# Kernel optimization log

Hardware: AMD Instinct MI355X
Metric: run time of the kernel (lower is better)

## Reference

```python
import jax, jax.numpy as jnp
import numpy as np

NUM_AGENTS = 1000
N_ACTIONS = 16
HIDDEN = 256
COMM_STEPS = 4
B, M = 1024, 64


def setup_inputs() -> dict:
    key = jax.random.key(0)
    ks = jax.random.split(key, 8)
    agent_ids = jax.random.randint(ks[0], (B, M), 0, NUM_AGENTS)
    emb = jax.random.normal(ks[1], (NUM_AGENTS, HIDDEN), dtype=jnp.float32) * 0.1
    s1 = 1.0 / np.sqrt(3 * HIDDEN)
    W1 = jax.random.uniform(ks[2], (3 * HIDDEN, HIDDEN), jnp.float32, -s1, s1)
    b1 = jax.random.uniform(ks[3], (HIDDEN,), jnp.float32, -s1, s1)
    s2 = 1.0 / np.sqrt(HIDDEN)
    W2 = jax.random.uniform(ks[4], (HIDDEN, HIDDEN), jnp.float32, -s2, s2)
    b2 = jax.random.uniform(ks[5], (HIDDEN,), jnp.float32, -s2, s2)
    Wd = jax.random.uniform(ks[6], (HIDDEN, N_ACTIONS), jnp.float32, -s2, s2)
    bd = jax.random.uniform(ks[7], (N_ACTIONS,), jnp.float32, -s2, s2)
    return {"agent_ids": agent_ids, "emb": emb, "W1": W1, "b1": b1,
            "W2": W2, "b2": b2, "Wd": Wd, "bd": bd}


def reference(agent_ids, emb, W1, b1, W2, b2, Wd, bd):
    # h0: (B, M, H) embedding lookup
    h0 = emb[agent_ids]
    h = h0
    m = agent_ids.shape[1]
    inv = 1.0 / (m - 1)
    for _ in range(COMM_STEPS):
        # mean of other agents' hidden states: c_j = (sum_k h_k - h_j)/(M-1)
        c = (jnp.sum(h, axis=1, keepdims=True) - h) * inv
        x = jnp.concatenate([h, c, h0], axis=-1)  # (B, M, 3H)
        delta = jax.nn.relu(jnp.einsum('bmi,ih->bmh', x, W1) + b1)
        delta = jnp.einsum('bmi,ih->bmh', delta, W2) + b2
        h = h + delta  # residual (use_skip=True)
    logits = jnp.einsum('bmh,ha->bma', h, Wd) + bd
    return logits
```

## Files before the change

kernel.cpp:

```cpp
#include <hip/hip_runtime.h>

#define HID 256
#define NB 1024
#define NACT 16
#define HSTRIDE 528

typedef __bf16 bf16x8 __attribute__((ext_vector_type(8)));
typedef float  f32x4  __attribute__((ext_vector_type(4)));

#define HA_LO   33792
#define HB_SZ   67584
#define S_OFF   135168
#define LDS_TOT 137216

#define PREP_N (4 * 65536 + 4096)

__device__ __forceinline__ unsigned short f2bf(float x) {
    union { __bf16 b; unsigned short u; } v; v.b = (__bf16)x; return v.u;
}
__device__ __forceinline__ float bf2f(unsigned short u) {
    union { unsigned short u; __bf16 b; } v; v.u = u; return (float)v.b;
}
__device__ __forceinline__ float b2f_lo(unsigned v) { return bf2f((unsigned short)(v & 0xffffu)); }
__device__ __forceinline__ float b2f_hi(unsigned v) { return bf2f((unsigned short)(v >> 16)); }
__device__ __forceinline__ unsigned pack2(float a, float b) {
    return (unsigned)f2bf(a) | ((unsigned)f2bf(b) << 16);
}

__global__ __launch_bounds__(256) void prep_k(const float* __restrict__ W1,
                                              const float* __restrict__ W2,
                                              const float* __restrict__ Wd,
                                              unsigned short* __restrict__ WAh, unsigned short* __restrict__ WAl,
                                              unsigned short* __restrict__ WHh, unsigned short* __restrict__ WHl,
                                              unsigned short* __restrict__ WBh, unsigned short* __restrict__ WBl,
                                              unsigned short* __restrict__ WCh, unsigned short* __restrict__ WCl,
                                              unsigned short* __restrict__ WDh, unsigned short* __restrict__ WDl) {
    int i = blockIdx.x * 256 + threadIdx.x;
    const float inv = 1.0f / 63.0f;
    if (i < 4 * 65536) {
        int mat = i >> 16, j = i & 65535;
        int kq = j >> 13, r = j & 8191;
        int nb = r >> 9, r2 = r & 511;
        int l = r2 >> 3, e = r2 & 7;
        int n = nb * 16 + (l & 15);
        int k = kq * 32 + (l >> 4) * 8 + e;
        float val;
        if (mat == 0)      val = W1[k * 256 + n] - inv * W1[(256 + k) * 256 + n];
        else if (mat == 1) val = W1[(512 + k) * 256 + n];
        else if (mat == 2) val = W2[k * 256 + n];
        else               val = inv * W1[(256 + k) * 256 + n];
        unsigned short hi = f2bf(val);
        unsigned short lo = f2bf(val - bf2f(hi));
        if (mat == 0)      { WAh[j] = hi; WAl[j] = lo; }
        else if (mat == 1) { WHh[j] = hi; WHl[j] = lo; }
        else if (mat == 2) { WBh[j] = hi; WBl[j] = lo; }
        else               { WCh[j] = hi; WCl[j] = lo; }
    } else if (i < PREP_N) {
        int j = i - 4 * 65536, a = j >> 8, k = j & 255;
        float val = Wd[k * 16 + a];
        unsigned short hi = f2bf(val);
        WDh[j] = hi; WDl[j] = f2bf(val - bf2f(hi));
    }
}

__device__ __forceinline__ void kloopL2(const unsigned short* __restrict__ Wfh,
                                        const unsigned short* __restrict__ Wfl,
                                        const char* hA, f32x4 (&acc)[4][2],
                                        size_t lbase, int l15, int g)
{
    #pragma unroll 2
    for (int kq = 0; kq < 8; ++kq) {
        const int cb = kq * 64 + g * 16;
        bf16x8 ah[4], al[4];
        #pragma unroll
        for (int mt = 0; mt < 4; ++mt) {
            int rb = (mt * 16 + l15) * HSTRIDE;
            ah[mt] = *(const bf16x8*)(hA + rb + cb);
            al[mt] = *(const bf16x8*)(hA + HA_LO + rb + cb);
        }
        const size_t kb = (size_t)kq * 8192 + lbase;
        #pragma unroll
        for (int nt = 0; nt < 2; ++nt) {
            bf16x8 bh = *(const bf16x8*)(Wfh + kb + nt * 512);
            bf16x8 bl = *(const bf16x8*)(Wfl + kb + nt * 512);
            #pragma unroll
            for (int mt = 0; mt < 4; ++mt) {
                acc[mt][nt] = __builtin_amdgcn_mfma_f32_16x16x32_bf16(bh, ah[mt], acc[mt][nt], 0, 0, 0);
                acc[mt][nt] = __builtin_amdgcn_mfma_f32_16x16x32_bf16(bh, al[mt], acc[mt][nt], 0, 0, 0);
                acc[mt][nt] = __builtin_amdgcn_mfma_f32_16x16x32_bf16(bl, ah[mt], acc[mt][nt], 0, 0, 0);
            }
        }
    }
}

__global__ __launch_bounds__(1024, 1) void fused_all(
    const int* __restrict__ ids, const float* __restrict__ emb,
    const unsigned short* __restrict__ WAh, const unsigned short* __restrict__ WAl,
    const unsigned short* __restrict__ WHh, const unsigned short* __restrict__ WHl,
    const unsigned short* __restrict__ WBh, const unsigned short* __restrict__ WBl,
    const unsigned short* __restrict__ WCh, const unsigned short* __restrict__ WCl,
    const unsigned short* __restrict__ WDh, const unsigned short* __restrict__ WDl,
    const float* __restrict__ b1, const float* __restrict__ b2,
    const float* __restrict__ bd, float* __restrict__ out)
{
    __shared__ __align__(16) char lds[LDS_TOT];
    const int tid = threadIdx.x;
    const int lane = tid & 63;
    const int w = tid >> 6;
    const int wcol = w & 7;
    const int batch = w >> 3;
    const int l15 = lane & 15, g = lane >> 4;
    const size_t rowbase = (size_t)blockIdx.x * 128 + batch * 64;
    char* hA = lds + batch * HB_SZ;
    float* Sf = (float*)(lds + S_OFF + batch * 1024);
    const size_t lbase = ((size_t)(wcol * 2) * 64 + lane) * 8;
    const int cb0 = wcol * 32 + g * 4;

    {
        int r = tid >> 3, c0 = (tid & 7) * 32;
        const float4* src = (const float4*)(emb + (size_t)ids[(size_t)blockIdx.x * 128 + r] * HID + c0);
        char* dh = lds + (r >> 6) * HB_SZ + (r & 63) * HSTRIDE + c0 * 2;
        #pragma unroll
        for (int j = 0; j < 8; ++j) {
            float4 v = src[j];
            unsigned short h0 = f2bf(v.x), h1 = f2bf(v.y), h2 = f2bf(v.z), h3 = f2bf(v.w);
            unsigned short q0 = f2bf(v.x - bf2f(h0)), q1 = f2bf(v.y - bf2f(h1)),
                           q2 = f2bf(v.z - bf2f(h2)), q3 = f2bf(v.w - bf2f(h3));
            *(uint2*)(dh + j * 8) = make_uint2((unsigned)h0 | ((unsigned)h1 << 16),
                                               (unsigned)h2 | ((unsigned)h3 << 16));
            *(uint2*)(dh + HA_LO + j * 8) = make_uint2((unsigned)q0 | ((unsigned)q1 << 16),
                                                       (unsigned)q2 | ((unsigned)q3 << 16));
        }
    }
    __syncthreads();

    if (tid < 512) {
        int b = tid >> 8, col = tid & 255;
        const char* hb = lds + b * HB_SZ;
        float ssum = 0.f;
        #pragma unroll 8
        for (int m = 0; m < 64; ++m) {
            int byte = m * HSTRIDE + col * 2;
            ssum += bf2f(*(const unsigned short*)(hb + byte))
                  + bf2f(*(const unsigned short*)(hb + HA_LO + byte));
        }
        ((float*)(lds + S_OFF + b * 1024))[col] = ssum;
    }
    __syncthreads();

    f32x4 b1v0 = *(const f32x4*)(b1 + cb0);
    f32x4 b1v1 = *(const f32x4*)(b1 + cb0 + 16);
    f32x4 b2v0 = *(const f32x4*)(b2 + cb0);
    f32x4 b2v1 = *(const f32x4*)(b2 + cb0 + 16);

    f32x4 acc[4][2], u0r[4][2];
    #pragma unroll
    for (int mt = 0; mt < 4; ++mt)
        #pragma unroll
        for (int nt = 0; nt < 2; ++nt) acc[mt][nt] = (f32x4){0.f, 0.f, 0.f, 0.f};

    kloopL2(WHh, WHl, hA, acc, lbase, l15, g);
    #pragma unroll
    for (int mt = 0; mt < 4; ++mt) {
        u0r[mt][0] = acc[mt][0] + b1v0;
        u0r[mt][1] = acc[mt][1] + b1v1;
    }

    for (int s = 0; s < 4; ++s) {
        f32x4 tacc[2];
        tacc[0] = tacc[1] = (f32x4){0.f, 0.f, 0.f, 0.f};
        #pragma unroll 2
        for (int kq = 0; kq < 8; ++kq) {
            const float* sp = Sf + kq * 32 + g * 8;
            f32x4 sa = *(const f32x4*)sp;
            f32x4 sb = *(const f32x4*)(sp + 4);
            unsigned sh[4], sl[4];
            sh[0] = pack2(sa[0], sa[1]); sh[1] = pack2(sa[2], sa[3]);
            sh[2] = pack2(sb[0], sb[1]); sh[3] = pack2(sb[2], sb[3]);
            sl[0] = pack2(sa[0] - b2f_lo(sh[0]), sa[1] - b2f_hi(sh[0]));
            sl[1] = pack2(sa[2] - b2f_lo(sh[1]), sa[3] - b2f_hi(sh[1]));
            sl[2] = pack2(sb[0] - b2f_lo(sh[2]), sb[1] - b2f_hi(sh[2]));
            sl[3] = pack2(sb[2] - b2f_lo(sh[3]), sb[3] - b2f_hi(sh[3]));
            bf16x8 shv = *(const bf16x8*)sh;
            bf16x8 slv = *(const bf16x8*)sl;
            const size_t kb = (size_t)kq * 8192 + lbase;
            #pragma unroll
            for (int nt = 0; nt < 2; ++nt) {
                bf16x8 wch = *(const bf16x8*)(WCh + kb + nt * 512);
                bf16x8 wcl = *(const bf16x8*)(WCl + kb + nt * 512);
                tacc[nt] = __builtin_amdgcn_mfma_f32_16x16x32_bf16(wch, shv, tacc[nt], 0, 0, 0);
                tacc[nt] = __builtin_amdgcn_mfma_f32_16x16x32_bf16(wch, slv, tacc[nt], 0, 0, 0);
                tacc[nt] = __builtin_amdgcn_mfma_f32_16x16x32_bf16(wcl, shv, tacc[nt], 0, 0, 0);
            }
        }

        #pragma unroll
        for (int mt = 0; mt < 4; ++mt)
            #pragma unroll
            for (int nt = 0; nt < 2; ++nt)
                acc[mt][nt] = u0r[mt][nt] + tacc[nt];
        kloopL2(WAh, WAl, hA, acc, lbase, l15, g);

        __syncthreads();
        #pragma unroll
        for (int mt = 0; mt < 4; ++mt)
            #pragma unroll
            for (int nt = 0; nt < 2; ++nt) {
                int byte = (mt * 16 + l15) * HSTRIDE + (cb0 + nt * 16) * 2;
                uint2 ph = *(const uint2*)(hA + byte);
                uint2 pl = *(const uint2*)(hA + HA_LO + byte);
                f32x4 hres;
                hres[0] = b2f_lo(ph.x) + b2f_lo(pl.x);
                hres[1] = b2f_hi(ph.x) + b2f_hi(pl.x);
                hres[2] = b2f_lo(ph.y) + b2f_lo(pl.y);
                hres[3] = b2f_hi(ph.y) + b2f_hi(pl.y);
                f32x4 av = acc[mt][nt];
                float a0 = fmaxf(av[0], 0.f), a1 = fmaxf(av[1], 0.f);
                float a2 = fmaxf(av[2], 0.f), a3 = fmaxf(av[3], 0.f);
                unsigned h01 = pack2(a0, a1), h23 = pack2(a2, a3);
                float r0 = a0 - b2f_lo(h01);
                float r1 = a1 - b2f_hi(h01);
                float r2 = a2 - b2f_lo(h23);
                float r3 = a3 - b2f_hi(h23);
                *(uint2*)(hA + byte) = make_uint2(h01, h23);
                *(uint2*)(hA + HA_LO + byte) = make_uint2(pack2(r0, r1), pack2(r2, r3));
                acc[mt][nt] = hres + (nt ? b2v1 : b2v0);
            }
        __syncthreads();

        kloopL2(WBh, WBl, hA, acc, lbase, l15, g);

        __syncthreads();
        #pragma unroll
        for (int mt = 0; mt < 4; ++mt)
            #pragma unroll
            for (int nt = 0; nt < 2; ++nt) {
                int byte = (mt * 16 + l15) * HSTRIDE + (cb0 + nt * 16) * 2;
                f32x4 av = acc[mt][nt];
                unsigned h01 = pack2(av[0], av[1]), h23 = pack2(av[2], av[3]);
                float r0 = av[0] - b2f_lo(h01);
                float r1 = av[1] - b2f_hi(h01);
                float r2 = av[2] - b2f_lo(h23);
                float r3 = av[3] - b2f_hi(h23);
                *(uint2*)(hA + byte) = make_uint2(h01, h23);
                *(uint2*)(hA + HA_LO + byte) = make_uint2(pack2(r0, r1), pack2(r2, r3));
            }
        if (s < 3) {
            #pragma unroll
            for (int nt = 0; nt < 2; ++nt) {
                f32x4 cs = (acc[0][nt] + acc[1][nt]) + (acc[2][nt] + acc[3][nt]);
                #pragma unroll
                for (int d = 1; d < 16; d <<= 1) {
                    cs[0] += __shfl_xor(cs[0], d);
                    cs[1] += __shfl_xor(cs[1], d);
                    cs[2] += __shfl_xor(cs[2], d);
                    cs[3] += __shfl_xor(cs[3], d);
                }
                if (l15 == 0) *(f32x4*)(Sf + cb0 + nt * 16) = cs;
            }
        }
        __syncthreads();
    }

    if (wcol < 4) {
        f32x4 dacc = (f32x4){0.f, 0.f, 0.f, 0.f};
        #pragma unroll 2
        for (int kq = 0; kq < 8; ++kq) {
            int byte = (wcol * 16 + l15) * HSTRIDE + kq * 64 + g * 16;
            bf16x8 hh = *(const bf16x8*)(hA + byte);
            bf16x8 hl = *(const bf16x8*)(hA + HA_LO + byte);
            const int k = kq * 32;
            bf16x8 wdh = *(const bf16x8*)(WDh + (size_t)l15 * 256 + k + g * 8);
            bf16x8 wdl = *(const bf16x8*)(WDl + (size_t)l15 * 256 + k + g * 8);
            dacc = __builtin_amdgcn_mfma_f32_16x16x32_bf16(wdh, hh, dacc, 0, 0, 0);
            dacc = __builtin_amdgcn_mfma_f32_16x16x32_bf16(wdh, hl, dacc, 0, 0, 0);
            dacc = __builtin_amdgcn_mfma_f32_16x16x32_bf16(wdl, hh, dacc, 0, 0, 0);
        }
        f32x4 bdv = *(const f32x4*)(bd + g * 4);
        f32x4 o = dacc + bdv;
        *(f32x4*)(out + (rowbase + wcol * 16 + l15) * NACT + g * 4) = o;
    }
}

extern "C" void kernel_launch(void* const* d_in, const int* in_sizes, int n_in,
                              void* d_out, int out_size, void* d_ws, size_t ws_size,
                              hipStream_t stream) {
    const int*   ids = (const int*)d_in[0];
    const float* emb = (const float*)d_in[1];
    const float* W1  = (const float*)d_in[2];
    const float* b1  = (const float*)d_in[3];
    const float* W2  = (const float*)d_in[4];
    const float* b2  = (const float*)d_in[5];
    const float* Wd  = (const float*)d_in[6];
    const float* bd  = (const float*)d_in[7];
    float* out = (float*)d_out;

    char* p = (char*)d_ws;
    unsigned short* WAh = (unsigned short*)p; p += 65536 * 2;
    unsigned short* WAl = (unsigned short*)p; p += 65536 * 2;
    unsigned short* WHh = (unsigned short*)p; p += 65536 * 2;
    unsigned short* WHl = (unsigned short*)p; p += 65536 * 2;
    unsigned short* WBh = (unsigned short*)p; p += 65536 * 2;
    unsigned short* WBl = (unsigned short*)p; p += 65536 * 2;
    unsigned short* WCh = (unsigned short*)p; p += 65536 * 2;
    unsigned short* WCl = (unsigned short*)p; p += 65536 * 2;
    unsigned short* WDh = (unsigned short*)p; p += 4096 * 2;
    unsigned short* WDl = (unsigned short*)p; p += 4096 * 2;

    prep_k<<<(PREP_N + 255) / 256, 256, 0, stream>>>(W1, W2, Wd, WAh, WAl, WHh, WHl,
                                                     WBh, WBl, WCh, WCl, WDh, WDl);
    fused_all<<<NB / 2, 1024, 0, stream>>>(ids, emb, WAh, WAl, WHh, WHl, WBh, WBl,
                                           WCh, WCl, WDh, WDl, b1, b2, bd, out);
}
```

Baseline: 267.6 us.

## Process one batch per block with two wave rows splitting the 64 agents

Each 1024-thread block now handles a single batch of 64 agents instead of two, with the 16 waves split into two row groups of 32 agents each. LDS per block drops by half and the grid doubles to 1024 blocks, which gives more blocks to spread across CUs and may let two blocks share a CU. Each wave holds half as many accumulators, and the column sums become two partial sums that are added when read. In exchange, each weight fragment loaded from global memory now feeds half as many MFMAs, so weight traffic per unit of work doubles.

```diff
diff --git a/kernel.cpp b/kernel.cpp
--- a/kernel.cpp
+++ b/kernel.cpp
@@ -9,9 +9,8 @@
 typedef float  f32x4  __attribute__((ext_vector_type(4)));
 
 #define HA_LO   33792
-#define HB_SZ   67584
-#define S_OFF   135168
-#define LDS_TOT 137216
+#define S_OFF   67584
+#define LDS_TOT 69632
 
 #define PREP_N (4 * 65536 + 4096)
 
@@ -65,18 +64,18 @@
 
 __device__ __forceinline__ void kloopL2(const unsigned short* __restrict__ Wfh,
                                         const unsigned short* __restrict__ Wfl,
-                                        const char* hA, f32x4 (&acc)[4][2],
+                                        const char* hW, f32x4 (&acc)[2][2],
                                         size_t lbase, int l15, int g)
 {
     #pragma unroll 2
     for (int kq = 0; kq < 8; ++kq) {
         const int cb = kq * 64 + g * 16;
-        bf16x8 ah[4], al[4];
-        #pragma unroll
-        for (int mt = 0; mt < 4; ++mt) {
+        bf16x8 ah[2], al[2];
+        #pragma unroll
+        for (int mt = 0; mt < 2; ++mt) {
             int rb = (mt * 16 + l15) * HSTRIDE;
-            ah[mt] = *(const bf16x8*)(hA + rb + cb);
-            al[mt] = *(const bf16x8*)(hA + HA_LO + rb + cb);
+            ah[mt] = *(const bf16x8*)(hW + rb + cb);
+            al[mt] = *(const bf16x8*)(hW + HA_LO + rb + cb);
         }
         const size_t kb = (size_t)kq * 8192 + lbase;
         #pragma unroll
@@ -84,7 +83,7 @@
             bf16x8 bh = *(const bf16x8*)(Wfh + kb + nt * 512);
             bf16x8 bl = *(const bf16x8*)(Wfl + kb + nt * 512);
             #pragma unroll
-            for (int mt = 0; mt < 4; ++mt) {
+            for (int mt = 0; mt < 2; ++mt) {
                 acc[mt][nt] = __builtin_amdgcn_mfma_f32_16x16x32_bf16(bh, ah[mt], acc[mt][nt], 0, 0, 0);
                 acc[mt][nt] = __builtin_amdgcn_mfma_f32_16x16x32_bf16(bh, al[mt], acc[mt][nt], 0, 0, 0);
                 acc[mt][nt] = __builtin_amdgcn_mfma_f32_16x16x32_bf16(bl, ah[mt], acc[mt][nt], 0, 0, 0);
@@ -108,20 +107,21 @@
     const int lane = tid & 63;
     const int w = tid >> 6;
     const int wcol = w & 7;
-    const int batch = w >> 3;
+    const int wrow = w >> 3;
     const int l15 = lane & 15, g = lane >> 4;
-    const size_t rowbase = (size_t)blockIdx.x * 128 + batch * 64;
-    char* hA = lds + batch * HB_SZ;
-    float* Sf = (float*)(lds + S_OFF + batch * 1024);
+    const size_t rowbase = (size_t)blockIdx.x * 64;
+    char* hA = lds;
+    char* hW = lds + wrow * 32 * HSTRIDE;
+    float* Sf = (float*)(lds + S_OFF);
     const size_t lbase = ((size_t)(wcol * 2) * 64 + lane) * 8;
     const int cb0 = wcol * 32 + g * 4;
 
     {
-        int r = tid >> 3, c0 = (tid & 7) * 32;
-        const float4* src = (const float4*)(emb + (size_t)ids[(size_t)blockIdx.x * 128 + r] * HID + c0);
-        char* dh = lds + (r >> 6) * HB_SZ + (r & 63) * HSTRIDE + c0 * 2;
-        #pragma unroll
-        for (int j = 0; j < 8; ++j) {
+        int r = tid >> 4, c0 = (tid & 15) * 16;
+        const float4* src = (const float4*)(emb + (size_t)ids[rowbase + r] * HID + c0);
+        char* dh = hA + r * HSTRIDE + c0 * 2;
+        #pragma unroll
+        for (int j = 0; j < 4; ++j) {
             float4 v = src[j];
             unsigned short h0 = f2bf(v.x), h1 = f2bf(v.y), h2 = f2bf(v.z), h3 = f2bf(v.w);
             unsigned short q0 = f2bf(v.x - bf2f(h0)), q1 = f2bf(v.y - bf2f(h1)),
@@ -135,16 +135,15 @@
     __syncthreads();
 
     if (tid < 512) {
-        int b = tid >> 8, col = tid & 255;
-        const char* hb = lds + b * HB_SZ;
+        int half = tid >> 8, col = tid & 255;
         float ssum = 0.f;
         #pragma unroll 8
-        for (int m = 0; m < 64; ++m) {
+        for (int m = half * 32; m < half * 32 + 32; ++m) {
             int byte = m * HSTRIDE + col * 2;
-            ssum += bf2f(*(const unsigned short*)(hb + byte))
-                  + bf2f(*(const unsigned short*)(hb + HA_LO + byte));
-        }
-        ((float*)(lds + S_OFF + b * 1024))[col] = ssum;
+            ssum += bf2f(*(const unsigned short*)(hA + byte))
+                  + bf2f(*(const unsigned short*)(hA + HA_LO + byte));
+        }
+        Sf[half * 256 + col] = ssum;
     }
     __syncthreads();
 
@@ -153,15 +152,15 @@
     f32x4 b2v0 = *(const f32x4*)(b2 + cb0);
     f32x4 b2v1 = *(const f32x4*)(b2 + cb0 + 16);
 
-    f32x4 acc[4][2], u0r[4][2];
+    f32x4 acc[2][2], u0r[2][2];
     #pragma unroll
-    for (int mt = 0; mt < 4; ++mt)
+    for (int mt = 0; mt < 2; ++mt)
         #pragma unroll
         for (int nt = 0; nt < 2; ++nt) acc[mt][nt] = (f32x4){0.f, 0.f, 0.f, 0.f};
 
-    kloopL2(WHh, WHl, hA, acc, lbase, l15, g);
+    kloopL2(WHh, WHl, hW, acc, lbase, l15, g);
     #pragma unroll
-    for (int mt = 0; mt < 4; ++mt) {
+    for (int mt = 0; mt < 2; ++mt) {
         u0r[mt][0] = acc[mt][0] + b1v0;
         u0r[mt][1] = acc[mt][1] + b1v1;
     }
@@ -171,9 +170,9 @@
         tacc[0] = tacc[1] = (f32x4){0.f, 0.f, 0.f, 0.f};
         #pragma unroll 2
         for (int kq = 0; kq < 8; ++kq) {
-            const float* sp = Sf + kq * 32 + g * 8;
-            f32x4 sa = *(const f32x4*)sp;
-            f32x4 sb = *(const f32x4*)(sp + 4);
+            const int c = kq * 32 + g * 8;
+            f32x4 sa = *(const f32x4*)(Sf + c)     + *(const f32x4*)(Sf + 256 + c);
+            f32x4 sb = *(const f32x4*)(Sf + c + 4) + *(const f32x4*)(Sf + 256 + c + 4);
             unsigned sh[4], sl[4];
             sh[0] = pack2(sa[0], sa[1]); sh[1] = pack2(sa[2], sa[3]);
             sh[2] = pack2(sb[0], sb[1]); sh[3] = pack2(sb[2], sb[3]);
@@ -195,20 +194,20 @@
         }
 
         #pragma unroll
-        for (int mt = 0; mt < 4; ++mt)
+        for (int mt = 0; mt < 2; ++mt)
             #pragma unroll
             for (int nt = 0; nt < 2; ++nt)
                 acc[mt][nt] = u0r[mt][nt] + tacc[nt];
-        kloopL2(WAh, WAl, hA, acc, lbase, l15, g);
+        kloopL2(WAh, WAl, hW, acc, lbase, l15, g);
 
         __syncthreads();
         #pragma unroll
-        for (int mt = 0; mt < 4; ++mt)
+        for (int mt = 0; mt < 2; ++mt)
             #pragma unroll
             for (int nt = 0; nt < 2; ++nt) {
                 int byte = (mt * 16 + l15) * HSTRIDE + (cb0 + nt * 16) * 2;
-                uint2 ph = *(const uint2*)(hA + byte);
-                uint2 pl = *(const uint2*)(hA + HA_LO + byte);
+                uint2 ph = *(const uint2*)(hW + byte);
+                uint2 pl = *(const uint2*)(hW + HA_LO + byte);
                 f32x4 hres;
                 hres[0] = b2f_lo(ph.x) + b2f_lo(pl.x);
                 hres[1] = b2f_hi(ph.x) + b2f_hi(pl.x);
@@ -222,17 +221,17 @@
                 float r1 = a1 - b2f_hi(h01);
                 float r2 = a2 - b2f_lo(h23);
                 float r3 = a3 - b2f_hi(h23);
-                *(uint2*)(hA + byte) = make_uint2(h01, h23);
-                *(uint2*)(hA + HA_LO + byte) = make_uint2(pack2(r0, r1), pack2(r2, r3));
+                *(uint2*)(hW + byte) = make_uint2(h01, h23);
+                *(uint2*)(hW + HA_LO + byte) = make_uint2(pack2(r0, r1), pack2(r2, r3));
                 acc[mt][nt] = hres + (nt ? b2v1 : b2v0);
             }
         __syncthreads();
 
-        kloopL2(WBh, WBl, hA, acc, lbase, l15, g);
+        kloopL2(WBh, WBl, hW, acc, lbase, l15, g);
 
         __syncthreads();
         #pragma unroll
-        for (int mt = 0; mt < 4; ++mt)
+        for (int mt = 0; mt < 2; ++mt)
             #pragma unroll
             for (int nt = 0; nt < 2; ++nt) {
                 int byte = (mt * 16 + l15) * HSTRIDE + (cb0 + nt * 16) * 2;
@@ -242,13 +241,13 @@
                 float r1 = av[1] - b2f_hi(h01);
                 float r2 = av[2] - b2f_lo(h23);
                 float r3 = av[3] - b2f_hi(h23);
-                *(uint2*)(hA + byte) = make_uint2(h01, h23);
-                *(uint2*)(hA + HA_LO + byte) = make_uint2(pack2(r0, r1), pack2(r2, r3));
+                *(uint2*)(hW + byte) = make_uint2(h01, h23);
+                *(uint2*)(hW + HA_LO + byte) = make_uint2(pack2(r0, r1), pack2(r2, r3));
             }
         if (s < 3) {
             #pragma unroll
             for (int nt = 0; nt < 2; ++nt) {
-                f32x4 cs = (acc[0][nt] + acc[1][nt]) + (acc[2][nt] + acc[3][nt]);
+                f32x4 cs = acc[0][nt] + acc[1][nt];
                 #pragma unroll
                 for (int d = 1; d < 16; d <<= 1) {
                     cs[0] += __shfl_xor(cs[0], d);
@@ -256,17 +255,17 @@
                     cs[2] += __shfl_xor(cs[2], d);
                     cs[3] += __shfl_xor(cs[3], d);
                 }
-                if (l15 == 0) *(f32x4*)(Sf + cb0 + nt * 16) = cs;
+                if (l15 == 0) *(f32x4*)(Sf + wrow * 256 + cb0 + nt * 16) = cs;
             }
         }
         __syncthreads();
     }
 
-    if (wcol < 4) {
+    if (w < 4) {
         f32x4 dacc = (f32x4){0.f, 0.f, 0.f, 0.f};
         #pragma unroll 2
         for (int kq = 0; kq < 8; ++kq) {
-            int byte = (wcol * 16 + l15) * HSTRIDE + kq * 64 + g * 16;
+            int byte = (w * 16 + l15) * HSTRIDE + kq * 64 + g * 16;
             bf16x8 hh = *(const bf16x8*)(hA + byte);
             bf16x8 hl = *(const bf16x8*)(hA + HA_LO + byte);
             const int k = kq * 32;
@@ -278,7 +277,7 @@
         }
         f32x4 bdv = *(const f32x4*)(bd + g * 4);
         f32x4 o = dacc + bdv;
-        *(f32x4*)(out + (rowbase + wcol * 16 + l15) * NACT + g * 4) = o;
+        *(f32x4*)(out + (rowbase + w * 16 + l15) * NACT + g * 4) = o;
     }
 }
 
@@ -309,6 +308,6 @@
 
     prep_k<<<(PREP_N + 255) / 256, 256, 0, stream>>>(W1, W2, Wd, WAh, WAl, WHh, WHl,
                                                      WBh, WBl, WCh, WCl, WDh, WDl);
-    fused_all<<<NB / 2, 1024, 0, stream>>>(ids, emb, WAh, WAl, WHh, WHl, WBh, WBl,
-                                           WCh, WCl, WDh, WDl, b1, b2, bd, out);
-}
+    fused_all<<<NB, 1024, 0, stream>>>(ids, emb, WAh, WAl, WHh, WHl, WBh, WBl,
+                                       WCh, WCl, WDh, WDl, b1, b2, bd, out);
+}
```

New measurement: 345.4 us. 29.1% more time.
